# Kernel optimization log

Measured on AMD Instinct MI355X. Metric: run time of the kernel, lower is better.

## Reference

```python
import jax, jax.numpy as jnp
import numpy as np

B, T = 2, 2048
D, H = 1024, 16
HD = D // H  # 64
L = 4
V = 32000
DFF = 4 * D
STD = 0.02


def layernorm(x, w, b, eps=1e-5):
    m = jnp.mean(x, axis=-1, keepdims=True)
    v = jnp.var(x, axis=-1, keepdims=True)
    return (x - m) / jnp.sqrt(v + eps) * w + b


def rope(x, cos, sin):
    # x: [B,H,T,HD]; cos/sin: [T, HD//2]
    xe = x[..., ::2]
    xo = x[..., 1::2]
    c = cos[None, None]
    s = sin[None, None]
    re = xe * c - xo * s
    ro = xe * s + xo * c
    return jnp.stack([re, ro], axis=-1).reshape(x.shape)


def setup_inputs() -> dict:
    key = jax.random.key(0)
    ks = jax.random.split(key, 16)
    n = lambda k, shp: jax.random.normal(k, shp, dtype=jnp.float32) * STD
    return {
        "idx": jax.random.randint(ks[0], (B, T), 0, V),
        "tok_emb": n(ks[1], (V, D)),
        "ln1_w": jnp.ones((L, D), jnp.float32),
        "ln1_b": jnp.zeros((L, D), jnp.float32),
        "Wq": n(ks[2], (L, D, D)),
        "Wk": n(ks[3], (L, D, D)),
        "Wv": n(ks[4], (L, D, D)),
        "Wp": n(ks[5], (L, D, D)),
        "ln2_w": jnp.ones((L, D), jnp.float32),
        "ln2_b": jnp.zeros((L, D), jnp.float32),
        "W1": n(ks[6], (L, D, DFF)),
        "b1": jnp.zeros((L, DFF), jnp.float32),
        "W2": n(ks[7], (L, DFF, D)),
        "b2": jnp.zeros((L, D), jnp.float32),
        "lnf_w": jnp.ones((D,), jnp.float32),
        "lnf_b": jnp.zeros((D,), jnp.float32),
    }


def reference(idx, tok_emb, ln1_w, ln1_b, Wq, Wk, Wv, Wp, ln2_w, ln2_b, W1, b1, W2, b2, lnf_w, lnf_b):
    x = tok_emb[idx]  # [B,T,D]
    # RoPE tables (base_freq=10000, no NTK since T == max_seq_len)
    freqs = 1.0 / (10000.0 ** (jnp.arange(0, HD, 2, dtype=jnp.float32) / HD))
    ang = jnp.arange(T, dtype=jnp.float32)[:, None] * freqs[None, :]  # [T, HD/2]
    cos, sin = jnp.cos(ang), jnp.sin(ang)
    causal = jnp.tril(jnp.ones((T, T), dtype=bool))

    def block(x, p):
        l1w, l1b, wq, wk, wv, wp, l2w, l2b, w1, bb1, w2, bb2 = p
        h = layernorm(x, l1w, l1b)
        q = (h @ wq).reshape(B, T, H, HD).transpose(0, 2, 1, 3)
        k = (h @ wk).reshape(B, T, H, HD).transpose(0, 2, 1, 3)
        v = (h @ wv).reshape(B, T, H, HD).transpose(0, 2, 1, 3)
        q = rope(q, cos, sin)
        k = rope(k, cos, sin)
        att = jnp.einsum('bhqd,bhkd->bhqk', q, k) / np.sqrt(HD).astype(np.float32)
        att = jnp.where(causal, att, -jnp.inf)
        att = jax.nn.softmax(att, axis=-1)
        y = jnp.einsum('bhqk,bhkd->bhqd', att, v)
        y = y.transpose(0, 2, 1, 3).reshape(B, T, D)
        x = x + y @ wp
        h2 = layernorm(x, l2w, l2b)
        # torch nn.GELU default = exact erf gelu
        x = x + (jax.nn.gelu(h2 @ w1 + bb1, approximate=False) @ w2 + bb2)
        return x, None

    params = (ln1_w, ln1_b, Wq, Wk, Wv, Wp, ln2_w, ln2_b, W1, b1, W2, b2)
    x, _ = jax.lax.scan(block, x, params)
    x = layernorm(x, lnf_w, lnf_b)
    logits = x @ tok_emb.T  # tied weights
    return logits
```

## Files before the change

### kernel.cpp

```cpp
#include <hip/hip_runtime.h>

#define Bv 2
#define Tv 2048
#define Dv 1024
#define Hv 16
#define HDv 64
#define Lv 4
#define Vv 32000
#define DFFv 4096
#define BTv (Bv * Tv)

typedef __attribute__((ext_vector_type(8))) short bfrag_t;
typedef __attribute__((ext_vector_type(4))) float f4_t;

__device__ __forceinline__ unsigned short f2bf(float f) {
  union { float f; unsigned int u; } cv; cv.f = f;
  unsigned int u = cv.u;
  u += 0x7fffu + ((u >> 16) & 1u);
  return (unsigned short)(u >> 16);
}

__global__ __launch_bounds__(256) void k_cvt(const float* __restrict__ src,
                                             unsigned short* __restrict__ dst, int n4) {
  int i = blockIdx.x * 256 + threadIdx.x;
  if (i >= n4) return;
  float4 v = ((const float4*)src)[i];
  ushort4 o;
  o.x = f2bf(v.x); o.y = f2bf(v.y); o.z = f2bf(v.z); o.w = f2bf(v.w);
  ((ushort4*)dst)[i] = o;
}

__global__ __launch_bounds__(256) void k_embed(const int* __restrict__ idx,
                                               const float* __restrict__ emb,
                                               float* __restrict__ x) {
  int row = blockIdx.x;
  ((float4*)(x + (size_t)row * Dv))[threadIdx.x] =
      ((const float4*)(emb + (size_t)idx[row] * Dv))[threadIdx.x];
}

__global__ __launch_bounds__(256) void k_tcvt(const float* __restrict__ src,
                                              unsigned short* __restrict__ dst,
                                              int R, int C) {
  __shared__ float tile[32][33];
  int c0 = blockIdx.x * 32, r0 = blockIdx.y * 32;
  int tx = threadIdx.x & 31, ty = threadIdx.x >> 5;
#pragma unroll
  for (int i = 0; i < 32; i += 8)
    tile[ty + i][tx] = src[(size_t)(r0 + ty + i) * C + c0 + tx];
  __syncthreads();
#pragma unroll
  for (int i = 0; i < 32; i += 8)
    dst[(size_t)(c0 + ty + i) * R + r0 + tx] = f2bf(tile[tx][ty + i]);
}

__global__ __launch_bounds__(256) void k_ln(const float* __restrict__ x,
                                            const float* __restrict__ w,
                                            const float* __restrict__ b,
                                            unsigned short* __restrict__ out) {
  int row = blockIdx.x, tid = threadIdx.x;
  float4 v = ((const float4*)(x + (size_t)row * Dv))[tid];
  float s = v.x + v.y + v.z + v.w;
  float s2 = v.x * v.x + v.y * v.y + v.z * v.z + v.w * v.w;
#pragma unroll
  for (int off = 32; off > 0; off >>= 1) {
    s += __shfl_xor(s, off);
    s2 += __shfl_xor(s2, off);
  }
  __shared__ float rs[4], rq[4];
  int wv_ = tid >> 6;
  if ((tid & 63) == 0) { rs[wv_] = s; rq[wv_] = s2; }
  __syncthreads();
  s = rs[0] + rs[1] + rs[2] + rs[3];
  s2 = rq[0] + rq[1] + rq[2] + rq[3];
  float mean = s * (1.0f / Dv);
  float var = s2 * (1.0f / Dv) - mean * mean;
  float rstd = rsqrtf(var + 1e-5f);
  float4 wv4 = ((const float4*)w)[tid];
  float4 bv4 = ((const float4*)b)[tid];
  ushort4 o;
  o.x = f2bf((v.x - mean) * rstd * wv4.x + bv4.x);
  o.y = f2bf((v.y - mean) * rstd * wv4.y + bv4.y);
  o.z = f2bf((v.z - mean) * rstd * wv4.z + bv4.z);
  o.w = f2bf((v.w - mean) * rstd * wv4.w + bv4.w);
  ((ushort4*)(out + (size_t)row * Dv))[tid] = o;
}

__global__ __launch_bounds__(256) void k_rope_cvt(const float* __restrict__ q,
                                                  const float* __restrict__ k,
                                                  unsigned short* __restrict__ qo,
                                                  unsigned short* __restrict__ ko) {
  int g = blockIdx.x * 256 + threadIdx.x;
  int row = g >> 9;
  int p = g & 511;
  int t = row & (Tv - 1);
  int hi = p & 31;
  float freq = (float)exp((double)hi * -0.28782313662425572);
  float ang = (float)t * freq;
  float sn, cs;
  sincosf(ang, &sn, &cs);
  size_t base = (size_t)row * Dv + (size_t)(p >> 5) * HDv + (size_t)hi * 2;
  float e = q[base], o = q[base + 1];
  qo[base] = f2bf((e * cs - o * sn) * 0.125f);
  qo[base + 1] = f2bf((e * sn + o * cs) * 0.125f);
  e = k[base]; o = k[base + 1];
  ko[base] = f2bf(e * cs - o * sn);
  ko[base + 1] = f2bf(e * sn + o * cs);
}

#define AST 72
__global__ __launch_bounds__(256) void k_attn(const unsigned short* __restrict__ q,
                                              const unsigned short* __restrict__ k,
                                              const unsigned short* __restrict__ v,
                                              unsigned short* __restrict__ y) {
  int qt = blockIdx.x, h = blockIdx.y, b = blockIdx.z;
  __shared__ unsigned short Ks[64 * AST];
  __shared__ unsigned short Vt[64 * AST];
  __shared__ unsigned short Ps[64 * AST];
  int tid = threadIdx.x;
  int lane = tid & 63, wave = tid >> 6;
  int lrow = lane & 15, lq = lane >> 4;

  size_t qbase = ((size_t)(b * Tv + qt * 64 + wave * 16 + lrow)) * Dv + h * HDv + lq * 8;
  bfrag_t aq0 = *(const bfrag_t*)(q + qbase);
  bfrag_t aq1 = *(const bfrag_t*)(q + qbase + 32);

  f4_t zero = {0.f, 0.f, 0.f, 0.f};
  f4_t o[4] = {zero, zero, zero, zero};
  float m[4] = {-1e30f, -1e30f, -1e30f, -1e30f};
  float l[4] = {0.f, 0.f, 0.f, 0.f};

  for (int kt = 0; kt <= qt; ++kt) {
    __syncthreads();
    size_t kvbase = ((size_t)(b * Tv + kt * 64)) * Dv + h * HDv;
#pragma unroll
    for (int it = 0; it < 2; ++it) {
      int id = tid + 256 * it;
      int key = id >> 3, d8 = (id & 7) * 8;
      *(bfrag_t*)&Ks[key * AST + d8] =
          *(const bfrag_t*)(k + kvbase + (size_t)key * Dv + d8);
      bfrag_t vv = *(const bfrag_t*)(v + kvbase + (size_t)key * Dv + d8);
#pragma unroll
      for (int j = 0; j < 8; ++j) Vt[(d8 + j) * AST + key] = (unsigned short)vv[j];
    }
    __syncthreads();

    f4_t sacc[4] = {zero, zero, zero, zero};
#pragma unroll
    for (int j = 0; j < 4; ++j) {
      bfrag_t kf0 = *(const bfrag_t*)&Ks[(j * 16 + lrow) * AST + lq * 8];
      bfrag_t kf1 = *(const bfrag_t*)&Ks[(j * 16 + lrow) * AST + 32 + lq * 8];
      sacc[j] = __builtin_amdgcn_mfma_f32_16x16x32_bf16(aq0, kf0, sacc[j], 0, 0, 0);
      sacc[j] = __builtin_amdgcn_mfma_f32_16x16x32_bf16(aq1, kf1, sacc[j], 0, 0, 0);
    }
    if (kt == qt) {
#pragma unroll
      for (int j = 0; j < 4; ++j)
#pragma unroll
        for (int r = 0; r < 4; ++r)
          if (lrow + 16 * j > wave * 16 + lq * 4 + r) sacc[j][r] = -1e30f;
    }

#pragma unroll
    for (int r = 0; r < 4; ++r) {
      float rmax = fmaxf(fmaxf(sacc[0][r], sacc[1][r]), fmaxf(sacc[2][r], sacc[3][r]));
#pragma unroll
      for (int msk = 1; msk < 16; msk <<= 1) rmax = fmaxf(rmax, __shfl_xor(rmax, msk));
      float mn = fmaxf(m[r], rmax);
      float alpha = expf(m[r] - mn);
      m[r] = mn;
      float psum = 0.f;
#pragma unroll
      for (int j = 0; j < 4; ++j) {
        float pv = expf(sacc[j][r] - mn);
        psum += pv;
        Ps[(wave * 16 + lq * 4 + r) * AST + lrow + 16 * j] = f2bf(pv);
      }
#pragma unroll
      for (int msk = 1; msk < 16; msk <<= 1) psum += __shfl_xor(psum, msk);
      l[r] = l[r] * alpha + psum;
      o[0][r] *= alpha; o[1][r] *= alpha; o[2][r] *= alpha; o[3][r] *= alpha;
    }
    __syncthreads();

    bfrag_t pf0 = *(const bfrag_t*)&Ps[(wave * 16 + lrow) * AST + lq * 8];
    bfrag_t pf1 = *(const bfrag_t*)&Ps[(wave * 16 + lrow) * AST + 32 + lq * 8];
#pragma unroll
    for (int dj = 0; dj < 4; ++dj) {
      bfrag_t vf0 = *(const bfrag_t*)&Vt[(dj * 16 + lrow) * AST + lq * 8];
      bfrag_t vf1 = *(const bfrag_t*)&Vt[(dj * 16 + lrow) * AST + 32 + lq * 8];
      o[dj] = __builtin_amdgcn_mfma_f32_16x16x32_bf16(pf0, vf0, o[dj], 0, 0, 0);
      o[dj] = __builtin_amdgcn_mfma_f32_16x16x32_bf16(pf1, vf1, o[dj], 0, 0, 0);
    }
  }

#pragma unroll
  for (int r = 0; r < 4; ++r) {
    float inv = 1.0f / l[r];
    size_t ybo = ((size_t)(b * Tv + qt * 64 + wave * 16 + lq * 4 + r)) * Dv + h * HDv;
#pragma unroll
    for (int dj = 0; dj < 4; ++dj)
      y[ybo + dj * 16 + lrow] = f2bf(o[dj][r] * inv);
  }
}

template <bool BIAS, bool RES, bool GELU, bool OUTF32, bool OUTBF16>
__global__ __launch_bounds__(256) void k_gemm(const unsigned short* __restrict__ A,
                                              const unsigned short* __restrict__ Bt,
                                              const float* __restrict__ bias,
                                              float* __restrict__ C,
                                              unsigned short* __restrict__ Cb,
                                              int M, int N, int K) {
  __shared__ unsigned short As[128 * 40];
  __shared__ unsigned short Bs[128 * 40];
  int tid = threadIdx.x;
  int n0 = blockIdx.x * 128, m0 = blockIdx.y * 128;
  int lane = tid & 63, wave = tid >> 6;
  int wm = (wave >> 1) * 64, wn = (wave & 1) * 64;
  int lrow = lane & 15, lq = lane >> 4;
  f4_t zero = {0.f, 0.f, 0.f, 0.f};
  f4_t acc[4][4];
#pragma unroll
  for (int i = 0; i < 4; ++i)
#pragma unroll
    for (int j = 0; j < 4; ++j) acc[i][j] = zero;
  int sr = tid >> 2, sq = (tid & 3) * 8;
  for (int kk = 0; kk < K; kk += 32) {
#pragma unroll
    for (int it = 0; it < 2; ++it) {
      int r = sr + it * 64;
      *(uint4*)(As + r * 40 + sq) = *(const uint4*)(A + (size_t)(m0 + r) * K + kk + sq);
      *(uint4*)(Bs + r * 40 + sq) = *(const uint4*)(Bt + (size_t)(n0 + r) * K + kk + sq);
    }
    __syncthreads();
    bfrag_t af[4], bfv[4];
#pragma unroll
    for (int i = 0; i < 4; ++i) {
      af[i] = *(const bfrag_t*)(As + (wm + i * 16 + lrow) * 40 + lq * 8);
      bfv[i] = *(const bfrag_t*)(Bs + (wn + i * 16 + lrow) * 40 + lq * 8);
    }
#pragma unroll
    for (int i = 0; i < 4; ++i)
#pragma unroll
      for (int j = 0; j < 4; ++j)
        acc[i][j] = __builtin_amdgcn_mfma_f32_16x16x32_bf16(af[i], bfv[j], acc[i][j], 0, 0, 0);
    __syncthreads();
  }
#pragma unroll
  for (int i = 0; i < 4; ++i) {
#pragma unroll
    for (int j = 0; j < 4; ++j) {
      int gc = n0 + wn + j * 16 + lrow;
      float bv = BIAS ? bias[gc] : 0.0f;
#pragma unroll
      for (int r = 0; r < 4; ++r) {
        int gr = m0 + wm + i * 16 + lq * 4 + r;
        float val = acc[i][j][r] + bv;
        if (GELU) val = 0.5f * val * (1.0f + erff(val * 0.70710678118654752f));
        size_t ci = (size_t)gr * N + gc;
        if (RES) val += C[ci];
        if (OUTF32) C[ci] = val;
        if (OUTBF16) Cb[ci] = f2bf(val);
      }
    }
  }
}

extern "C" void kernel_launch(void* const* d_in, const int* in_sizes, int n_in,
                              void* d_out, int out_size, void* d_ws, size_t ws_size,
                              hipStream_t stream) {
  const int* idx = (const int*)d_in[0];
  const float* tok = (const float*)d_in[1];
  const float* ln1w = (const float*)d_in[2];
  const float* ln1b = (const float*)d_in[3];
  const float* Wq = (const float*)d_in[4];
  const float* Wk = (const float*)d_in[5];
  const float* Wv = (const float*)d_in[6];
  const float* Wp = (const float*)d_in[7];
  const float* ln2w = (const float*)d_in[8];
  const float* ln2b = (const float*)d_in[9];
  const float* W1 = (const float*)d_in[10];
  const float* b1 = (const float*)d_in[11];
  const float* W2 = (const float*)d_in[12];
  const float* b2 = (const float*)d_in[13];
  const float* lnfw = (const float*)d_in[14];
  const float* lnfb = (const float*)d_in[15];
  float* out = (float*)d_out;

  char* ws = (char*)d_ws;
  size_t off = 0;
  auto alloc = [&](size_t bytes) -> void* {
    void* p = ws + off;
    off += (bytes + 255) & ~(size_t)255;
    return p;
  };
  float* x = (float*)alloc((size_t)BTv * Dv * 4);
  unsigned short* hb = (unsigned short*)alloc((size_t)BTv * Dv * 2);
  float* qb = (float*)alloc((size_t)BTv * Dv * 4);
  float* kb = (float*)alloc((size_t)BTv * Dv * 4);
  unsigned short* yb = (unsigned short*)alloc((size_t)BTv * Dv * 2);
  unsigned short* ub = (unsigned short*)alloc((size_t)BTv * DFFv * 2);
  unsigned short* wqt = (unsigned short*)alloc((size_t)Dv * Dv * 2);
  unsigned short* wkt = (unsigned short*)alloc((size_t)Dv * Dv * 2);
  unsigned short* wvt = (unsigned short*)alloc((size_t)Dv * Dv * 2);
  unsigned short* wpt = (unsigned short*)alloc((size_t)Dv * Dv * 2);
  unsigned short* w1t = (unsigned short*)alloc((size_t)DFFv * Dv * 2);
  unsigned short* w2t = (unsigned short*)alloc((size_t)Dv * DFFv * 2);
  unsigned short* embb = (unsigned short*)alloc((size_t)Vv * Dv * 2);
  unsigned short* qb16 = ub;
  unsigned short* kb16 = ub + (size_t)BTv * Dv;
  unsigned short* vb16 = ub + (size_t)2 * BTv * Dv;

  k_cvt<<<(Vv * Dv / 4 + 255) / 256, 256, 0, stream>>>(tok, embb, Vv * Dv / 4);
  k_embed<<<BTv, 256, 0, stream>>>(idx, tok, x);
  for (int l = 0; l < Lv; ++l) {
    k_tcvt<<<dim3(Dv / 32, Dv / 32), 256, 0, stream>>>(Wq + (size_t)l * Dv * Dv, wqt, Dv, Dv);
    k_tcvt<<<dim3(Dv / 32, Dv / 32), 256, 0, stream>>>(Wk + (size_t)l * Dv * Dv, wkt, Dv, Dv);
    k_tcvt<<<dim3(Dv / 32, Dv / 32), 256, 0, stream>>>(Wv + (size_t)l * Dv * Dv, wvt, Dv, Dv);
    k_tcvt<<<dim3(Dv / 32, Dv / 32), 256, 0, stream>>>(Wp + (size_t)l * Dv * Dv, wpt, Dv, Dv);
    k_tcvt<<<dim3(DFFv / 32, Dv / 32), 256, 0, stream>>>(W1 + (size_t)l * Dv * DFFv, w1t, Dv, DFFv);
    k_tcvt<<<dim3(Dv / 32, DFFv / 32), 256, 0, stream>>>(W2 + (size_t)l * DFFv * Dv, w2t, DFFv, Dv);
    k_ln<<<BTv, 256, 0, stream>>>(x, ln1w + l * Dv, ln1b + l * Dv, hb);
    k_gemm<false, false, false, true, false><<<dim3(Dv / 128, BTv / 128), 256, 0, stream>>>(
        hb, wqt, nullptr, qb, nullptr, BTv, Dv, Dv);
    k_gemm<false, false, false, true, false><<<dim3(Dv / 128, BTv / 128), 256, 0, stream>>>(
        hb, wkt, nullptr, kb, nullptr, BTv, Dv, Dv);
    k_gemm<false, false, false, false, true><<<dim3(Dv / 128, BTv / 128), 256, 0, stream>>>(
        hb, wvt, nullptr, nullptr, vb16, BTv, Dv, Dv);
    k_rope_cvt<<<(BTv * 512) / 256, 256, 0, stream>>>(qb, kb, qb16, kb16);
    k_attn<<<dim3(Tv / 64, Hv, Bv), 256, 0, stream>>>(qb16, kb16, vb16, yb);
    k_gemm<false, true, false, true, false><<<dim3(Dv / 128, BTv / 128), 256, 0, stream>>>(
        yb, wpt, nullptr, x, nullptr, BTv, Dv, Dv);
    k_ln<<<BTv, 256, 0, stream>>>(x, ln2w + l * Dv, ln2b + l * Dv, hb);
    k_gemm<true, false, true, false, true><<<dim3(DFFv / 128, BTv / 128), 256, 0, stream>>>(
        hb, w1t, b1 + l * DFFv, nullptr, ub, BTv, DFFv, Dv);
    k_gemm<true, true, false, true, false><<<dim3(Dv / 128, BTv / 128), 256, 0, stream>>>(
        ub, w2t, b2 + l * Dv, x, nullptr, BTv, Dv, DFFv);
  }
  k_ln<<<BTv, 256, 0, stream>>>(x, lnfw, lnfb, hb);
  k_gemm<false, false, false, true, false><<<dim3(Vv / 128, BTv / 128), 256, 0, stream>>>(
      hb, embb, nullptr, out, nullptr, BTv, Vv, Dv);
  (void)in_sizes; (void)n_in; (void)out_size; (void)ws_size;
}
```

Before: 3.185 ms.

## Fuse QKV GEMMs, load GEMM tiles via global_load_lds, add XCD-aware tile swizzle

```diff
diff --git a/kernel.cpp b/kernel.cpp
--- a/kernel.cpp
+++ b/kernel.cpp
@@ -9,6 +9,7 @@
 #define Vv 32000
 #define DFFv 4096
 #define BTv (Bv * Tv)
+#define D3v 3072
 
 typedef __attribute__((ext_vector_type(8))) short bfrag_t;
 typedef __attribute__((ext_vector_type(4))) float f4_t;
@@ -18,6 +19,11 @@
   unsigned int u = cv.u;
   u += 0x7fffu + ((u >> 16) & 1u);
   return (unsigned short)(u >> 16);
+}
+
+__device__ __forceinline__ void gload16(const void* g, void* l) {
+  __builtin_amdgcn_global_load_lds((__attribute__((address_space(1))) void*)g,
+                                   (__attribute__((address_space(3))) void*)l, 16, 0, 0);
 }
 
 __global__ __launch_bounds__(256) void k_cvt(const float* __restrict__ src,
@@ -85,8 +91,7 @@
   ((ushort4*)(out + (size_t)row * Dv))[tid] = o;
 }
 
-__global__ __launch_bounds__(256) void k_rope_cvt(const float* __restrict__ q,
-                                                  const float* __restrict__ k,
+__global__ __launch_bounds__(256) void k_rope_cvt(const float* __restrict__ qkv,
                                                   unsigned short* __restrict__ qo,
                                                   unsigned short* __restrict__ ko) {
   int g = blockIdx.x * 256 + threadIdx.x;
@@ -98,13 +103,24 @@
   float ang = (float)t * freq;
   float sn, cs;
   sincosf(ang, &sn, &cs);
-  size_t base = (size_t)row * Dv + (size_t)(p >> 5) * HDv + (size_t)hi * 2;
-  float e = q[base], o = q[base + 1];
-  qo[base] = f2bf((e * cs - o * sn) * 0.125f);
-  qo[base + 1] = f2bf((e * sn + o * cs) * 0.125f);
-  e = k[base]; o = k[base + 1];
-  ko[base] = f2bf(e * cs - o * sn);
-  ko[base + 1] = f2bf(e * sn + o * cs);
+  size_t ibase = (size_t)row * D3v + (size_t)(p >> 5) * HDv + (size_t)hi * 2;
+  size_t obase = (size_t)row * Dv + (size_t)(p >> 5) * HDv + (size_t)hi * 2;
+  float e = qkv[ibase], o = qkv[ibase + 1];
+  qo[obase] = f2bf((e * cs - o * sn) * 0.125f);
+  qo[obase + 1] = f2bf((e * sn + o * cs) * 0.125f);
+  e = qkv[ibase + Dv]; o = qkv[ibase + Dv + 1];
+  ko[obase] = f2bf(e * cs - o * sn);
+  ko[obase + 1] = f2bf(e * sn + o * cs);
+}
+
+__global__ __launch_bounds__(256) void k_vcvt(const float* __restrict__ qkv,
+                                              unsigned short* __restrict__ vo) {
+  int i = blockIdx.x * 256 + threadIdx.x;
+  int row = i >> 8, c4 = (i & 255) * 4;
+  float4 v = *(const float4*)(qkv + (size_t)row * D3v + 2 * Dv + c4);
+  ushort4 o;
+  o.x = f2bf(v.x); o.y = f2bf(v.y); o.z = f2bf(v.z); o.w = f2bf(v.w);
+  *(ushort4*)(vo + (size_t)row * Dv + c4) = o;
 }
 
 #define AST 72
@@ -210,11 +226,25 @@
                                               float* __restrict__ C,
                                               unsigned short* __restrict__ Cb,
                                               int M, int N, int K) {
-  __shared__ unsigned short As[128 * 40];
-  __shared__ unsigned short Bs[128 * 40];
+  __shared__ unsigned short As[128 * 32];
+  __shared__ unsigned short Bs[128 * 32];
   int tid = threadIdx.x;
-  int n0 = blockIdx.x * 128, m0 = blockIdx.y * 128;
   int lane = tid & 63, wave = tid >> 6;
+
+  int nbx = gridDim.x, nby = gridDim.y;
+  int bid = blockIdx.y * nbx + blockIdx.x;
+  int nwg = nbx * nby;
+  int q8 = nwg >> 3, r8 = nwg & 7;
+  int xcd = bid & 7, loc = bid >> 3;
+  int swz = (xcd < r8 ? xcd * (q8 + 1) : r8 * (q8 + 1) + (xcd - r8) * q8) + loc;
+  int panel = 8 * nby;
+  int pid = swz / panel;
+  int rem = swz - pid * panel;
+  int pw = nbx - pid * 8; if (pw > 8) pw = 8;
+  int mt = rem / pw;
+  int nt = pid * 8 + rem - mt * pw;
+  int n0 = nt * 128, m0 = mt * 128;
+
   int wm = (wave >> 1) * 64, wn = (wave & 1) * 64;
   int lrow = lane & 15, lq = lane >> 4;
   f4_t zero = {0.f, 0.f, 0.f, 0.f};
@@ -223,20 +253,23 @@
   for (int i = 0; i < 4; ++i)
 #pragma unroll
     for (int j = 0; j < 4; ++j) acc[i][j] = zero;
-  int sr = tid >> 2, sq = (tid & 3) * 8;
+
+  int srow_l = lane >> 2;
+  int sc = (lane & 3) * 8;
   for (int kk = 0; kk < K; kk += 32) {
 #pragma unroll
     for (int it = 0; it < 2; ++it) {
-      int r = sr + it * 64;
-      *(uint4*)(As + r * 40 + sq) = *(const uint4*)(A + (size_t)(m0 + r) * K + kk + sq);
-      *(uint4*)(Bs + r * 40 + sq) = *(const uint4*)(Bt + (size_t)(n0 + r) * K + kk + sq);
+      int seg = wave + 4 * it;
+      int srow = seg * 16 + srow_l;
+      gload16(A + (size_t)(m0 + srow) * K + kk + sc, &As[seg * 512]);
+      gload16(Bt + (size_t)(n0 + srow) * K + kk + sc, &Bs[seg * 512]);
     }
     __syncthreads();
     bfrag_t af[4], bfv[4];
 #pragma unroll
     for (int i = 0; i < 4; ++i) {
-      af[i] = *(const bfrag_t*)(As + (wm + i * 16 + lrow) * 40 + lq * 8);
-      bfv[i] = *(const bfrag_t*)(Bs + (wn + i * 16 + lrow) * 40 + lq * 8);
+      af[i] = *(const bfrag_t*)(As + (wm + i * 16 + lrow) * 32 + lq * 8);
+      bfv[i] = *(const bfrag_t*)(Bs + (wn + i * 16 + lrow) * 32 + lq * 8);
     }
 #pragma unroll
     for (int i = 0; i < 4; ++i)
@@ -295,13 +328,10 @@
   };
   float* x = (float*)alloc((size_t)BTv * Dv * 4);
   unsigned short* hb = (unsigned short*)alloc((size_t)BTv * Dv * 2);
-  float* qb = (float*)alloc((size_t)BTv * Dv * 4);
-  float* kb = (float*)alloc((size_t)BTv * Dv * 4);
+  float* qkvb = (float*)alloc((size_t)BTv * D3v * 4);
   unsigned short* yb = (unsigned short*)alloc((size_t)BTv * Dv * 2);
   unsigned short* ub = (unsigned short*)alloc((size_t)BTv * DFFv * 2);
-  unsigned short* wqt = (unsigned short*)alloc((size_t)Dv * Dv * 2);
-  unsigned short* wkt = (unsigned short*)alloc((size_t)Dv * Dv * 2);
-  unsigned short* wvt = (unsigned short*)alloc((size_t)Dv * Dv * 2);
+  unsigned short* wqkvt = (unsigned short*)alloc((size_t)D3v * Dv * 2);
   unsigned short* wpt = (unsigned short*)alloc((size_t)Dv * Dv * 2);
   unsigned short* w1t = (unsigned short*)alloc((size_t)DFFv * Dv * 2);
   unsigned short* w2t = (unsigned short*)alloc((size_t)Dv * DFFv * 2);
@@ -313,20 +343,20 @@
   k_cvt<<<(Vv * Dv / 4 + 255) / 256, 256, 0, stream>>>(tok, embb, Vv * Dv / 4);
   k_embed<<<BTv, 256, 0, stream>>>(idx, tok, x);
   for (int l = 0; l < Lv; ++l) {
-    k_tcvt<<<dim3(Dv / 32, Dv / 32), 256, 0, stream>>>(Wq + (size_t)l * Dv * Dv, wqt, Dv, Dv);
-    k_tcvt<<<dim3(Dv / 32, Dv / 32), 256, 0, stream>>>(Wk + (size_t)l * Dv * Dv, wkt, Dv, Dv);
-    k_tcvt<<<dim3(Dv / 32, Dv / 32), 256, 0, stream>>>(Wv + (size_t)l * Dv * Dv, wvt, Dv, Dv);
+    k_tcvt<<<dim3(Dv / 32, Dv / 32), 256, 0, stream>>>(Wq + (size_t)l * Dv * Dv,
+                                                       wqkvt, Dv, Dv);
+    k_tcvt<<<dim3(Dv / 32, Dv / 32), 256, 0, stream>>>(Wk + (size_t)l * Dv * Dv,
+                                                       wqkvt + (size_t)Dv * Dv, Dv, Dv);
+    k_tcvt<<<dim3(Dv / 32, Dv / 32), 256, 0, stream>>>(Wv + (size_t)l * Dv * Dv,
+                                                       wqkvt + (size_t)2 * Dv * Dv, Dv, Dv);
     k_tcvt<<<dim3(Dv / 32, Dv / 32), 256, 0, stream>>>(Wp + (size_t)l * Dv * Dv, wpt, Dv, Dv);
     k_tcvt<<<dim3(DFFv / 32, Dv / 32), 256, 0, stream>>>(W1 + (size_t)l * Dv * DFFv, w1t, Dv, DFFv);
     k_tcvt<<<dim3(Dv / 32, DFFv / 32), 256, 0, stream>>>(W2 + (size_t)l * DFFv * Dv, w2t, DFFv, Dv);
     k_ln<<<BTv, 256, 0, stream>>>(x, ln1w + l * Dv, ln1b + l * Dv, hb);
-    k_gemm<false, false, false, true, false><<<dim3(Dv / 128, BTv / 128), 256, 0, stream>>>(
-        hb, wqt, nullptr, qb, nullptr, BTv, Dv, Dv);
-    k_gemm<false, false, false, true, false><<<dim3(Dv / 128, BTv / 128), 256, 0, stream>>>(
-        hb, wkt, nullptr, kb, nullptr, BTv, Dv, Dv);
-    k_gemm<false, false, false, false, true><<<dim3(Dv / 128, BTv / 128), 256, 0, stream>>>(
-        hb, wvt, nullptr, nullptr, vb16, BTv, Dv, Dv);
-    k_rope_cvt<<<(BTv * 512) / 256, 256, 0, stream>>>(qb, kb, qb16, kb16);
+    k_gemm<false, false, false, true, false><<<dim3(D3v / 128, BTv / 128), 256, 0, stream>>>(
+        hb, wqkvt, nullptr, qkvb, nullptr, BTv, D3v, Dv);
+    k_rope_cvt<<<(BTv * 512) / 256, 256, 0, stream>>>(qkvb, qb16, kb16);
+    k_vcvt<<<BTv, 256, 0, stream>>>(qkvb, vb16);
     k_attn<<<dim3(Tv / 64, Hv, Bv), 256, 0, stream>>>(qb16, kb16, vb16, yb);
     k_gemm<false, true, false, true, false><<<dim3(Dv / 128, BTv / 128), 256, 0, stream>>>(
         yb, wpt, nullptr, x, nullptr, BTv, Dv, Dv);
```

After: 2.929 ms. -8.1%, faster.
